# Kernel optimization log

Measured on AMD Instinct MI355X. Metric: run time of the kernel, lower is better.

## Reference

```python
import jax, jax.numpy as jnp
import numpy as np

N_E = 1024
E_DIM = 256
BETA = 0.25
EPS = 1e-10


def setup_inputs() -> dict:
    key = jax.random.key(0)
    k1, k2 = jax.random.split(key)
    z = jax.random.normal(k1, (32, E_DIM, 32, 32), dtype=jnp.float32)
    emb = jax.random.normal(k2, (N_E, E_DIM), dtype=jnp.float32)
    return {"z": z, "emb": emb}


def reference(z, emb):
    sg = jax.lax.stop_gradient
    # (B, C, H, W) -> (B, H, W, C)
    zp = jnp.transpose(z, (0, 2, 3, 1))
    zf = zp.reshape(-1, E_DIM)  # (N, C), N = B*H*W
    # squared euclidean distances: ||z||^2 + ||e||^2 - 2 z e^T  -> (N, n_e)
    d = (jnp.sum(zf * zf, axis=1, keepdims=True)
         + jnp.sum(emb * emb, axis=1)
         - 2.0 * jnp.matmul(zf, emb.T))
    idx = jnp.argmin(d, axis=1)  # (N,)
    # one-hot @ codebook == gather (same math, no dense one-hot matmul)
    z_q1 = emb[idx].reshape(zp.shape)  # (B, H, W, C)
    # loss: note original does NOT detach z_q1 anywhere
    loss = jnp.mean((z_q1 - zp) ** 2) + BETA * jnp.mean((z_q1 - sg(zp)) ** 2)
    # straight-through (original detaches z, not z_q1)
    z_q = zp + (z_q1 - sg(zp))
    # perplexity from mean one-hot encodings = normalized histogram of indices
    counts = jnp.bincount(idx, length=N_E)
    e_mean = counts.astype(zf.dtype) / idx.shape[0]
    perplexity = jnp.exp(-jnp.sum(e_mean * jnp.log(e_mean + EPS)))
    z_q = jnp.transpose(z_q, (0, 3, 1, 2))
    z_q1_out = jnp.transpose(z_q1, (0, 3, 1, 2))
    return loss, z_q, perplexity, idx, z_q1_out
```

## Files before the change

### kernel.cpp

```cpp
#include <hip/hip_runtime.h>
#include <hip/hip_bf16.h>
#include <math.h>

#define CDIM 256
#define HW   1024
#define NVEC 32768
#define NE   1024
#define ZSIZE 8388608
#define NSPLIT 4
#define MARGIN 0.12f
#define ZPCAP 15360

#define OUT_LOSS 0
#define OUT_ZQ   1
#define OUT_PERP 8388609
#define OUT_IDX  8388610
#define OUT_ZQ1  8421378

#define WS_LOSS   0
#define WS_RCNT   64
#define WS_GCNT   96
#define WS_MCNT   128
#define WS_HIST   1152
#define WS_ENORM  5248
#define WS_IDX    9472
#define WS_RLIST  140544
#define WS_S1     271616
#define WS_S2     795904
#define WS_J1     1320192
#define WS_SCORE  1844480
#define WS_EBH    2106624
#define WS_ZBH    2630912
#define WS_ZPACK  19408128
#define WS_LPART  35136768
#define WS_ZERO_INTS 1312

typedef __attribute__((ext_vector_type(8))) short short8;
typedef __attribute__((ext_vector_type(4))) float f32x4;
typedef __attribute__((ext_vector_type(8))) unsigned short ushort8v;
typedef __attribute__((ext_vector_type(8))) _Float16 half8;

__device__ __forceinline__ unsigned short f16_rne(float x) {
    _Float16 h = (_Float16)x;
    return __builtin_bit_cast(unsigned short, h);
}
__device__ __forceinline__ void lds_barrier() {
    asm volatile("s_waitcnt lgkmcnt(0)\n\ts_barrier" ::: "memory");
}

__global__ __launch_bounds__(256) void vq_prep(
    const float* __restrict__ z, const float* __restrict__ emb,
    unsigned short* __restrict__ zbh, unsigned short* __restrict__ ebh,
    float* __restrict__ enorm, int* __restrict__ wsz)
{
    const int tid = threadIdx.x, w = tid >> 6, L = tid & 63;
    if (blockIdx.x < 512) {
        __shared__ unsigned short th[64 * 264];
        const int b = blockIdx.x >> 4, hw0 = (blockIdx.x & 15) << 6;
        const float* zp = z + (size_t)b * (CDIM * HW) + hw0;
        for (int i = 0; i < 16; ++i) {
            int k = (i * 4 + w) * 4;
            float f0 = zp[(size_t)(k + 0) * HW + L];
            float f1 = zp[(size_t)(k + 1) * HW + L];
            float f2 = zp[(size_t)(k + 2) * HW + L];
            float f3 = zp[(size_t)(k + 3) * HW + L];
            ushort4 hi = { f16_rne(f0), f16_rne(f1), f16_rne(f2), f16_rne(f3) };
            *(ushort4*)&th[L * 264 + k] = hi;
        }
        __syncthreads();
#pragma unroll
        for (int it = 0; it < 8; ++it) {
            int row = it * 8 + (tid >> 5);
            int kc = (tid & 31) * 8;
            size_t o = (size_t)(b * 1024 + hw0 + row) * CDIM + kc;
            *(ushort8v*)(zbh + o) = *(ushort8v*)&th[row * 264 + kc];
        }
    } else {
        if (blockIdx.x == 512) {
            for (int i = tid; i < WS_ZERO_INTS; i += 256) wsz[i] = 0;
        }
        const int cb = (int)(blockIdx.x - 512) * 64;
        for (int p = 0; p < 16; ++p) {
            int code = cb + p * 4 + w;
            float4 v = *(const float4*)(emb + (size_t)code * CDIM + L * 4);
            float s = v.x * v.x + v.y * v.y + v.z * v.z + v.w * v.w;
            for (int off = 32; off; off >>= 1) s += __shfl_down(s, off, 64);
            if (L == 0) enorm[code] = s;
            ushort4 hi = { f16_rne(v.x), f16_rne(v.y), f16_rne(v.z), f16_rne(v.w) };
            *(ushort4*)(ebh + (size_t)code * CDIM + L * 4) = hi;
        }
    }
}

__global__ __launch_bounds__(256, 3) void vq_mfma3(
    const unsigned short* __restrict__ zbh, const unsigned short* __restrict__ ebh,
    const float* __restrict__ enorm,
    float* __restrict__ s1_ws, float* __restrict__ s2_ws, int* __restrict__ j1_ws)
{
    __shared__ short bpan[32 * 512];
    __shared__ float en_s[256];

    const int tid = threadIdx.x, w = tid >> 6, L = tid & 63;
    const int l15 = L & 15, q = L >> 4;
    const int r16 = tid & 15, ch = (tid >> 4) & 3;
    const int mtile = blockIdx.x & 255, js = blockIdx.x >> 8;
    const int n0 = mtile << 7;
    const int jsbase = js << 8;

    half8 AH[2][8];
#pragma unroll
    for (int mf = 0; mf < 2; ++mf)
#pragma unroll
        for (int kk = 0; kk < 8; ++kk)
            AH[mf][kk] = *(const half8*)(zbh + (size_t)(n0 + w * 32 + mf * 16 + l15) * CDIM + kk * 32 + q * 8);

    en_s[tid] = enorm[jsbase + tid];

    float s1[2][4], s2[2][4]; int j1v[2][4];
#pragma unroll
    for (int mf = 0; mf < 2; ++mf)
#pragma unroll
        for (int r = 0; r < 4; ++r) { s1[mf][r] = -3.4e38f; s2[mf][r] = -3.4e38f; j1v[mf][r] = 0; }

    const unsigned short* ebase = ebh + (size_t)(jsbase + w * 16 + r16) * CDIM + ch * 8;

    short8 st[8];
#pragma unroll
    for (int kk = 0; kk < 8; ++kk) st[kk] = *(const short8*)(ebase + kk * 32);
#pragma unroll
    for (int kk = 0; kk < 8; ++kk) *(short8*)(bpan + (w * 8 + kk) * 512 + L * 8) = st[kk];
#pragma unroll
    for (int kk = 0; kk < 8; ++kk) st[kk] = *(const short8*)(ebase + 64 * CDIM + kk * 32);
    lds_barrier();

    for (int p = 0; p < 4; ++p) {
        f32x4 acc[2][4] = {};
#pragma unroll
        for (int kk = 0; kk < 8; ++kk) {
#pragma unroll
            for (int jf = 0; jf < 4; ++jf) {
                half8 B = *(const half8*)(bpan + (jf * 8 + kk) * 512 + L * 8);
                acc[0][jf] = __builtin_amdgcn_mfma_f32_16x16x32_f16(AH[0][kk], B, acc[0][jf], 0, 0, 0);
                acc[1][jf] = __builtin_amdgcn_mfma_f32_16x16x32_f16(AH[1][kk], B, acc[1][jf], 0, 0, 0);
            }
        }
#pragma unroll
        for (int jf = 0; jf < 4; ++jf) {
            const int jl = p * 64 + jf * 16 + l15;
            const int j = jsbase + jl;
            const float hn = 0.5f * en_s[jl];
#pragma unroll
            for (int mf = 0; mf < 2; ++mf)
#pragma unroll
                for (int r = 0; r < 4; ++r) {
                    float s = acc[mf][jf][r] - hn;
                    if (s > s1[mf][r]) { s2[mf][r] = s1[mf][r]; s1[mf][r] = s; j1v[mf][r] = j; }
                    else if (s > s2[mf][r]) s2[mf][r] = s;
                }
        }
        if (p < 3) {
            lds_barrier();
#pragma unroll
            for (int kk = 0; kk < 8; ++kk) *(short8*)(bpan + (w * 8 + kk) * 512 + L * 8) = st[kk];
            if (p < 2) {
#pragma unroll
                for (int kk = 0; kk < 8; ++kk)
                    st[kk] = *(const short8*)(ebase + (size_t)(p + 2) * 64 * CDIM + kk * 32);
            }
            lds_barrier();
        }
    }

#pragma unroll
    for (int mf = 0; mf < 2; ++mf)
#pragma unroll
        for (int r = 0; r < 4; ++r) {
            float a1 = s1[mf][r], a2 = s2[mf][r]; int aj = j1v[mf][r];
            for (int m = 1; m < 16; m <<= 1) {
                float o1 = __shfl_xor(a1, m, 64);
                float o2 = __shfl_xor(a2, m, 64);
                int   oj = __shfl_xor(aj, m, 64);
                if (o1 > a1 || (o1 == a1 && oj < aj)) { a2 = fmaxf(a1, o2); a1 = o1; aj = oj; }
                else a2 = fmaxf(a2, o1);
            }
            if (l15 == 0) {
                int o = js * NVEC + n0 + w * 32 + mf * 16 + q * 4 + r;
                s1_ws[o] = a1; s2_ws[o] = a2; j1_ws[o] = aj;
            }
        }
}

__global__ __launch_bounds__(256) void vq_merge(
    const float* __restrict__ s1_ws, const float* __restrict__ s2_ws,
    const int* __restrict__ j1_ws, int* __restrict__ idx_ws,
    float* __restrict__ idx_out, int* __restrict__ hist,
    int* __restrict__ rcnt, int* __restrict__ rlist,
    unsigned long long* __restrict__ score)
{
    int n = blockIdx.x * 256 + threadIdx.x;
    score[n] = 0ull;
    float b1 = -3.4e38f, b2 = -3.4e38f; int bj = 0;
#pragma unroll
    for (int s = 0; s < NSPLIT; ++s) {
        float a1 = s1_ws[s * NVEC + n], a2 = s2_ws[s * NVEC + n];
        int aj = j1_ws[s * NVEC + n];
        if (a1 > b1 || (a1 == b1 && aj < bj)) { b2 = fmaxf(b1, a2); b1 = a1; bj = aj; }
        else b2 = fmaxf(b2, a1);
    }
    if (b1 - b2 < MARGIN) {
        idx_ws[n] = -1;
        int p = atomicAdd(rcnt, 1); rlist[p] = n;
    } else {
        idx_ws[n] = bj;
        idx_out[n] = (float)bj;
        atomicAdd(&hist[bj], 1);
    }
}

__global__ __launch_bounds__(256) void vq_zpack(
    const float* __restrict__ z, const int* __restrict__ rcnt,
    const int* __restrict__ rlist, float* __restrict__ zpack)
{
    const int count = min(*rcnt, ZPCAP);
    for (int it = blockIdx.x; it < count; it += gridDim.x) {
        const int n = rlist[it];
        zpack[(size_t)it * 256 + threadIdx.x] =
            z[(size_t)(n >> 10) * (CDIM * HW) + (size_t)threadIdx.x * HW + (n & 1023)];
    }
}

__global__ __launch_bounds__(256) void vq_rescue(
    const float* __restrict__ z, const float* __restrict__ emb,
    const float* __restrict__ enorm, const int* __restrict__ rcnt,
    const int* __restrict__ rlist, const float* __restrict__ zpack,
    unsigned long long* __restrict__ score)
{
    __shared__ float en_s[64];
    __shared__ __align__(16) float zrow[256];
    __shared__ float rs[4];
    __shared__ int   rj[4];
    const int tid = threadIdx.x;
    const int wv = tid >> 6, L = tid & 63;
    const int chunk = blockIdx.x & 15;
    const int jwave = chunk * 64 + wv * 16;
    const int jodd = L >> 5;
    const int rstride = gridDim.x >> 4;
    const int count = *rcnt;

    if (tid < 64) en_s[tid] = enorm[chunk * 64 + tid];
    __syncthreads();

    for (int it = blockIdx.x >> 4; it < count; it += rstride) {
        const int n = rlist[it];
        float4 zv;
        if (it < ZPCAP) {
            zv = *(const float4*)(zpack + (size_t)it * 256 + L * 4);
        } else {
            __syncthreads();
            zrow[tid] = z[(size_t)(n >> 10) * (CDIM * HW) + (size_t)tid * HW + (n & 1023)];
            __syncthreads();
            zv = *(const float4*)&zrow[L * 4];
        }

        float b1 = -3.4e38f; int bj = 0x7fffffff;
#pragma unroll
        for (int jo = 0; jo < 16; jo += 2) {
            const int jA = jwave + jo;
            const float4 eA = *(const float4*)(emb + (size_t)jA * CDIM + L * 4);
            const float4 eB = *(const float4*)(emb + (size_t)(jA + 1) * CDIM + L * 4);
            float pA = fmaf(zv.x, eA.x, fmaf(zv.y, eA.y, fmaf(zv.z, eA.z, zv.w * eA.w)));
            float pB = fmaf(zv.x, eB.x, fmaf(zv.y, eB.y, fmaf(zv.z, eB.z, zv.w * eB.w)));
            float tA = pA + __shfl_xor(pA, 32, 64);
            float tB = pB + __shfl_xor(pB, 32, 64);
            float u = (L < 32) ? tA : tB;
            u += __shfl_xor(u, 16, 64);
            u += __shfl_xor(u, 8, 64);
            u += __shfl_xor(u, 4, 64);
            u += __shfl_xor(u, 2, 64);
            u += __shfl_xor(u, 1, 64);
            const int j = jA + jodd;
            const float s = u - 0.5f * en_s[wv * 16 + jo + jodd];
            if (s > b1) { b1 = s; bj = j; }
        }
        {
            const float o1 = __shfl_xor(b1, 32, 64);
            const int   oj = __shfl_xor(bj, 32, 64);
            if (o1 > b1 || (o1 == b1 && oj < bj)) { b1 = o1; bj = oj; }
        }
        __syncthreads();
        if (L == 0) { rs[wv] = b1; rj[wv] = bj; }
        __syncthreads();
        if (tid == 0) {
            float f1 = rs[0]; int fj = rj[0];
#pragma unroll
            for (int v = 1; v < 4; ++v)
                if (rs[v] > f1 || (rs[v] == f1 && rj[v] < fj)) { f1 = rs[v]; fj = rj[v]; }
            unsigned key = __float_as_uint(f1);
            key = (key & 0x80000000u) ? ~key : (key | 0x80000000u);
            unsigned long long packed = ((unsigned long long)key << 32) | (unsigned)(~fj);
            atomicMax(&score[n], packed);
        }
    }
}

__global__ __launch_bounds__(256) void vq_gather(
    const float* __restrict__ z, const float* __restrict__ emb,
    const int* __restrict__ idx_ws, const unsigned long long* __restrict__ score,
    float* __restrict__ zq, float* __restrict__ zq1,
    float* __restrict__ idx_out, int* __restrict__ hist,
    float* __restrict__ loss_part)
{
    __shared__ float es[32 * 129];
    __shared__ int ids[32];
    __shared__ float wred[4];

    const int tid = threadIdx.x, w = tid >> 6, L = tid & 63;
    const int b   = blockIdx.x >> 6;
    const int half = (blockIdx.x >> 5) & 1;
    const int hw0 = (blockIdx.x & 31) << 5;
    const int n0  = (b << 10) + hw0;
    const int c0  = half << 7;

    if (tid < 32) {
        const int n = n0 + tid;
        int id = idx_ws[n];
        if (id < 0) {
            id = (int)(~(unsigned)score[n]) & (NE - 1);
            if (half == 0) {
                idx_out[n] = (float)id;
                atomicAdd(&hist[id], 1);
            }
        }
        ids[tid] = id;
    }
    __syncthreads();

#pragma unroll
    for (int p = 0; p < 4; ++p) {
        int u = p * 256 + tid;
        int r = u >> 5, cq = (u & 31) * 4;
        float4 v = *(const float4*)(emb + (size_t)ids[r] * CDIM + c0 + cq);
        es[r * 129 + cq + 0] = v.x;
        es[r * 129 + cq + 1] = v.y;
        es[r * 129 + cq + 2] = v.z;
        es[r * 129 + cq + 3] = v.w;
    }
    __syncthreads();

    const int row = L & 31, cp = L >> 5;
    const size_t zbase = (size_t)b * (CDIM * HW) + hw0 + row;
    float ls = 0.f;
    for (int rd = 0; rd < 16; ++rd) {
        int cl = rd * 8 + w * 2 + cp;
        size_t off = zbase + (size_t)(c0 + cl) * HW;
        float zv = z[off];
        float e  = es[row * 129 + cl];
        float d  = e - zv;
        zq[off]  = zv + d;
        zq1[off] = e;
        ls += d * d;
    }

    for (int off = 32; off; off >>= 1) ls += __shfl_down(ls, off, 64);
    if (L == 0) wred[w] = ls;
    __syncthreads();
    if (tid == 0)
        loss_part[blockIdx.x] = wred[0] + wred[1] + wred[2] + wred[3];
}

__global__ __launch_bounds__(1024) void vq_final(
    const int* __restrict__ hist, const float* __restrict__ loss_part,
    float* __restrict__ out_loss, float* __restrict__ out_perp)
{
    int tid = threadIdx.x;
    float em = (float)hist[tid] * (1.0f / 32768.0f);
    float term = em * logf(em + 1e-10f);
    double dl = (double)loss_part[tid] + (double)loss_part[tid + 1024];
    for (int off = 32; off; off >>= 1) {
        term += __shfl_down(term, off, 64);
        dl   += __shfl_down(dl, off, 64);
    }
    __shared__ float red[16];
    __shared__ double redd[16];
    int lane = tid & 63, wv = tid >> 6;
    if (lane == 0) { red[wv] = term; redd[wv] = dl; }
    __syncthreads();
    if (tid == 0) {
        float s = 0.f; double dsum = 0.0;
        for (int i = 0; i < 16; ++i) { s += red[i]; dsum += redd[i]; }
        *out_perp = expf(-s);
        *out_loss = (float)(dsum * 1.25 / 8388608.0);
    }
}

extern "C" void kernel_launch(void* const* d_in, const int* in_sizes, int n_in,
                              void* d_out, int out_size, void* d_ws, size_t ws_size,
                              hipStream_t stream) {
    const float* z   = (const float*)d_in[0];
    const float* emb = (const float*)d_in[1];
    float* out = (float*)d_out;
    char*  ws  = (char*)d_ws;

    int*    rcnt        = (int*)(ws + WS_RCNT);
    int*    hist        = (int*)(ws + WS_HIST);
    float*  enorm       = (float*)(ws + WS_ENORM);
    int*    idx_ws      = (int*)(ws + WS_IDX);
    int*    rlist       = (int*)(ws + WS_RLIST);
    float*  s1_ws       = (float*)(ws + WS_S1);
    float*  s2_ws       = (float*)(ws + WS_S2);
    int*    j1_ws       = (int*)(ws + WS_J1);
    unsigned short* ebh = (unsigned short*)(ws + WS_EBH);
    unsigned short* zbh = (unsigned short*)(ws + WS_ZBH);
    float*  zpack       = (float*)(ws + WS_ZPACK);
    float*  loss_part   = (float*)(ws + WS_LPART);
    unsigned long long* score = (unsigned long long*)(ws + WS_SCORE);

    vq_prep  <<<528, 256, 0, stream>>>(z, emb, zbh, ebh, enorm, (int*)ws);
    vq_mfma3 <<<1024, 256, 0, stream>>>(zbh, ebh, enorm, s1_ws, s2_ws, j1_ws);
    vq_merge <<<128, 256, 0, stream>>>(s1_ws, s2_ws, j1_ws, idx_ws, out + OUT_IDX, hist, rcnt, rlist, score);
    vq_zpack <<<1024, 256, 0, stream>>>(z, rcnt, rlist, zpack);
    vq_rescue<<<2048, 256, 0, stream>>>(z, emb, enorm, rcnt, rlist, zpack, score);
    vq_gather<<<2048, 256, 0, stream>>>(z, emb, idx_ws, score, out + OUT_ZQ, out + OUT_ZQ1,
                                        out + OUT_IDX, hist, loss_part);
    vq_final <<<1, 1024, 0, stream>>>(hist, loss_part, out + OUT_LOSS, out + OUT_PERP);
}
```

Baseline: 233.4 us.

## Double-buffer codebook panels via direct global-to-LDS loads in distance kernel

Measured after the change: 229.6 us. About the same (-1.6%).

```diff
diff --git a/kernel.cpp b/kernel.cpp
--- a/kernel.cpp
+++ b/kernel.cpp
@@ -47,6 +47,11 @@
 __device__ __forceinline__ void lds_barrier() {
     asm volatile("s_waitcnt lgkmcnt(0)\n\ts_barrier" ::: "memory");
 }
+__device__ __forceinline__ void gload_lds16(const unsigned short* g, unsigned short* l) {
+    __builtin_amdgcn_global_load_lds(
+        (const __attribute__((address_space(1))) unsigned int*)g,
+        (__attribute__((address_space(3))) unsigned int*)l, 16, 0, 0);
+}
 
 __global__ __launch_bounds__(256) void vq_prep(
     const float* __restrict__ z, const float* __restrict__ emb,
@@ -92,17 +97,17 @@
     }
 }
 
-__global__ __launch_bounds__(256, 3) void vq_mfma3(
+__global__ __launch_bounds__(256, 4) void vq_mfma3(
     const unsigned short* __restrict__ zbh, const unsigned short* __restrict__ ebh,
     const float* __restrict__ enorm,
     float* __restrict__ s1_ws, float* __restrict__ s2_ws, int* __restrict__ j1_ws)
 {
-    __shared__ short bpan[32 * 512];
+    __shared__ unsigned short bpan[2][8192];
     __shared__ float en_s[256];
 
     const int tid = threadIdx.x, w = tid >> 6, L = tid & 63;
     const int l15 = L & 15, q = L >> 4;
-    const int r16 = tid & 15, ch = (tid >> 4) & 3;
+    const int r16 = tid & 15;
     const int mtile = blockIdx.x & 255, js = blockIdx.x >> 8;
     const int n0 = mtile << 7;
     const int jsbase = js << 8;
@@ -122,31 +127,41 @@
 #pragma unroll
         for (int r = 0; r < 4; ++r) { s1[mf][r] = -3.4e38f; s2[mf][r] = -3.4e38f; j1v[mf][r] = 0; }
 
-    const unsigned short* ebase = ebh + (size_t)(jsbase + w * 16 + r16) * CDIM + ch * 8;
-
-    short8 st[8];
-#pragma unroll
-    for (int kk = 0; kk < 8; ++kk) st[kk] = *(const short8*)(ebase + kk * 32);
-#pragma unroll
-    for (int kk = 0; kk < 8; ++kk) *(short8*)(bpan + (w * 8 + kk) * 512 + L * 8) = st[kk];
-#pragma unroll
-    for (int kk = 0; kk < 8; ++kk) st[kk] = *(const short8*)(ebase + 64 * CDIM + kk * 32);
-    lds_barrier();
-
-    for (int p = 0; p < 4; ++p) {
-        f32x4 acc[2][4] = {};
+    const int jf_st = w >> 1;
+    const int kk0 = (w & 1) * 4;
+    const unsigned short* gsrc0 = ebh + (size_t)(jsbase + jf_st * 16 + r16) * CDIM + kk0 * 32 + q * 8;
+    unsigned short* ldst0 = &bpan[0][(w * 4) * 512];
+    unsigned short* ldst1 = &bpan[1][(w * 4) * 512];
+
+#define ISSUE_PANEL(pp, ld)                                     \
+    {                                                           \
+        const unsigned short* gs = gsrc0 + (size_t)(pp) * 32 * CDIM; \
+        gload_lds16(gs,      (ld));                             \
+        gload_lds16(gs + 32, (ld) + 512);                       \
+        gload_lds16(gs + 64, (ld) + 1024);                      \
+        gload_lds16(gs + 96, (ld) + 1536);                      \
+    }
+
+    ISSUE_PANEL(0, ldst0);
+    ISSUE_PANEL(1, ldst1);
+    __syncthreads();
+
+#pragma unroll 2
+    for (int p = 0; p < 8; ++p) {
+        const unsigned short* bb = bpan[p & 1];
+        f32x4 acc[2][2] = {};
 #pragma unroll
         for (int kk = 0; kk < 8; ++kk) {
 #pragma unroll
-            for (int jf = 0; jf < 4; ++jf) {
-                half8 B = *(const half8*)(bpan + (jf * 8 + kk) * 512 + L * 8);
+            for (int jf = 0; jf < 2; ++jf) {
+                half8 B = *(const half8*)(bb + (jf * 8 + kk) * 512 + L * 8);
                 acc[0][jf] = __builtin_amdgcn_mfma_f32_16x16x32_f16(AH[0][kk], B, acc[0][jf], 0, 0, 0);
                 acc[1][jf] = __builtin_amdgcn_mfma_f32_16x16x32_f16(AH[1][kk], B, acc[1][jf], 0, 0, 0);
             }
         }
 #pragma unroll
-        for (int jf = 0; jf < 4; ++jf) {
-            const int jl = p * 64 + jf * 16 + l15;
+        for (int jf = 0; jf < 2; ++jf) {
+            const int jl = p * 32 + jf * 16 + l15;
             const int j = jsbase + jl;
             const float hn = 0.5f * en_s[jl];
 #pragma unroll
@@ -158,18 +173,13 @@
                     else if (s > s2[mf][r]) s2[mf][r] = s;
                 }
         }
-        if (p < 3) {
-            lds_barrier();
-#pragma unroll
-            for (int kk = 0; kk < 8; ++kk) *(short8*)(bpan + (w * 8 + kk) * 512 + L * 8) = st[kk];
-            if (p < 2) {
-#pragma unroll
-                for (int kk = 0; kk < 8; ++kk)
-                    st[kk] = *(const short8*)(ebase + (size_t)(p + 2) * 64 * CDIM + kk * 32);
-            }
-            lds_barrier();
-        }
-    }
+        __syncthreads();
+        if (p < 6) {
+            unsigned short* ld = (p & 1) ? ldst1 : ldst0;
+            ISSUE_PANEL(p + 2, ld);
+        }
+    }
+#undef ISSUE_PANEL
 
 #pragma unroll
     for (int mf = 0; mf < 2; ++mf)
```
